# Kernel tuning notes

Hardware: AMD Instinct MI355X
Metric: run time of the kernel (lower is better)

## Reference

```python
import jax, jax.numpy as jnp
import numpy as np

N_NODES = 100000
IN_DIM = 128
OUT_DIM = 128
N_EDGES = 1000000
ALPHA = 0.2  # LeakyReLU negative slope


def _xavier(key, shape):
    gain = 1.414
    bound = gain * np.sqrt(6.0 / (shape[0] + shape[1]))
    return jax.random.uniform(key, shape, jnp.float32, -bound, bound)


def setup_inputs() -> dict:
    key = jax.random.key(0)
    ks = jax.random.split(key, 10)
    return {
        "disease_feats": jax.random.normal(ks[0], (N_NODES, IN_DIM), jnp.float32),
        "gene_feats": jax.random.normal(ks[1], (N_NODES, IN_DIM), jnp.float32),
        "chemical_feats": jax.random.normal(ks[2], (N_NODES, IN_DIM), jnp.float32),
        "species_feats": jax.random.normal(ks[3], (N_NODES, IN_DIM), jnp.float32),
        "trans_adj_list": jax.random.randint(ks[4], (4, N_EDGES), 0, N_NODES, jnp.int32),
        "P_disease": _xavier(ks[5], (IN_DIM, OUT_DIM)),
        "P_gene": _xavier(ks[6], (IN_DIM, OUT_DIM)),
        "P_chemical": _xavier(ks[7], (IN_DIM, OUT_DIM)),
        "P_species": _xavier(ks[8], (IN_DIM, OUT_DIM)),
        "W_GDCD": _xavier(ks[9], (4 * OUT_DIM, OUT_DIM)),
    }


def reference(disease_feats, gene_feats, chemical_feats, species_feats,
              trans_adj_list, P_disease, P_gene, P_chemical, P_species, W_GDCD):
    # pattern_name == 'GDCD'
    f_disease = disease_feats @ P_disease      # [N, D]
    f_gene = gene_feats @ P_gene
    f_chemical = chemical_feats @ P_chemical
    f_species = species_feats @ P_species      # computed as in original (unused for GDCD output)
    concat = jnp.concatenate([
        f_disease[trans_adj_list[0]],          # [E, D]
        f_disease[trans_adj_list[1]],
        f_gene[trans_adj_list[2]],
        f_chemical[trans_adj_list[3]],
    ], axis=1)                                 # [E, 4D]
    instance = jax.nn.leaky_relu(concat @ W_GDCD, negative_slope=ALPHA)
    return instance
```

## Files before the change

kernel.cpp:

```cpp
#include <hip/hip_runtime.h>
#include <hip/hip_fp16.h>


#define DIM 128
#define ALPHA 0.2f

__global__ __launch_bounds__(128) void compute_M(
    const float* __restrict__ Pd, const float* __restrict__ Pg,
    const float* __restrict__ Pc, const float* __restrict__ W,
    float* __restrict__ M) {
    const int i = blockIdx.x;
    const int k = blockIdx.y;
    const int j = threadIdx.x;
    const float* P = (k < 2) ? Pd : (k == 2 ? Pg : Pc);
    __shared__ float prow[DIM];
    prow[j] = P[i * DIM + j];
    __syncthreads();
    const float* Wb = W + k * DIM * DIM;
    float acc = 0.f;
#pragma unroll 8
    for (int t = 0; t < DIM; ++t)
        acc = fmaf(prow[t], Wb[t * DIM + j], acc);
    M[(k * DIM + i) * DIM + j] = acc;
}

#define BM 64
#define BK 32
__global__ __launch_bounds__(256) void node_gemm(
    const float* __restrict__ Fd, const float* __restrict__ Fg,
    const float* __restrict__ Fc, const float* __restrict__ M,
    __half* __restrict__ H, int nNodes) {
    const int k = blockIdx.y;
    const float* F = (k < 2) ? Fd : (k == 2 ? Fg : Fc);
    const float* Mk = M + k * DIM * DIM;
    __half* Hk = H + (size_t)k * nNodes * DIM;
    const int row0 = blockIdx.x * BM;

    __shared__ float As[BM][BK + 1];
    __shared__ float Bs[BK][DIM];

    const int t = threadIdx.x;
    const int tc = t & 15;
    const int tr = t >> 4;

    float acc[4][8];
#pragma unroll
    for (int i = 0; i < 4; ++i)
#pragma unroll
        for (int j = 0; j < 8; ++j) acc[i][j] = 0.f;

    for (int kk = 0; kk < DIM; kk += BK) {
#pragma unroll
        for (int q = 0; q < 2; ++q) {
            int l = q * 256 + t;
            int r = l >> 3;
            int c4 = l & 7;
            int grow = row0 + r;
            float4 v = make_float4(0.f, 0.f, 0.f, 0.f);
            if (grow < nNodes)
                v = *reinterpret_cast<const float4*>(F + (size_t)grow * DIM + kk + c4 * 4);
            As[r][c4 * 4 + 0] = v.x;
            As[r][c4 * 4 + 1] = v.y;
            As[r][c4 * 4 + 2] = v.z;
            As[r][c4 * 4 + 3] = v.w;
        }
#pragma unroll
        for (int q = 0; q < 4; ++q) {
            int l = q * 256 + t;
            int r = l >> 5;
            int c4 = l & 31;
            *reinterpret_cast<float4*>(&Bs[r][c4 * 4]) =
                *reinterpret_cast<const float4*>(Mk + (size_t)(kk + r) * DIM + c4 * 4);
        }
        __syncthreads();
#pragma unroll
        for (int kki = 0; kki < BK; ++kki) {
            float a[4];
#pragma unroll
            for (int i = 0; i < 4; ++i) a[i] = As[tr * 4 + i][kki];
            float4 b0 = *reinterpret_cast<float4*>(&Bs[kki][tc * 4]);
            float4 b1 = *reinterpret_cast<float4*>(&Bs[kki][64 + tc * 4]);
#pragma unroll
            for (int i = 0; i < 4; ++i) {
                acc[i][0] = fmaf(a[i], b0.x, acc[i][0]);
                acc[i][1] = fmaf(a[i], b0.y, acc[i][1]);
                acc[i][2] = fmaf(a[i], b0.z, acc[i][2]);
                acc[i][3] = fmaf(a[i], b0.w, acc[i][3]);
                acc[i][4] = fmaf(a[i], b1.x, acc[i][4]);
                acc[i][5] = fmaf(a[i], b1.y, acc[i][5]);
                acc[i][6] = fmaf(a[i], b1.z, acc[i][6]);
                acc[i][7] = fmaf(a[i], b1.w, acc[i][7]);
            }
        }
        __syncthreads();
    }
#pragma unroll
    for (int i = 0; i < 4; ++i) {
        int row = row0 + tr * 4 + i;
        if (row < nNodes) {
            union { __half2 h[4]; uint2 u[2]; } p;
            p.h[0] = __floats2half2_rn(acc[i][0], acc[i][1]);
            p.h[1] = __floats2half2_rn(acc[i][2], acc[i][3]);
            p.h[2] = __floats2half2_rn(acc[i][4], acc[i][5]);
            p.h[3] = __floats2half2_rn(acc[i][6], acc[i][7]);
            *reinterpret_cast<uint2*>(Hk + (size_t)row * DIM + tc * 4) = p.u[0];
            *reinterpret_cast<uint2*>(Hk + (size_t)row * DIM + 64 + tc * 4) = p.u[1];
        }
    }
}

__device__ __forceinline__ float4 load_h4(const __half* __restrict__ p) {
    float2 r = *reinterpret_cast<const float2*>(p);
    const __half2* h = reinterpret_cast<const __half2*>(&r);
    float2 lo = __half22float2(h[0]);
    float2 hi = __half22float2(h[1]);
    return make_float4(lo.x, lo.y, hi.x, hi.y);
}

__global__ __launch_bounds__(256) void edge_agg(
    const int* __restrict__ adj, const __half* __restrict__ H,
    float* __restrict__ out, int nEdges, int nNodes) {
    __shared__ int idx[32];
    const int e0 = blockIdx.x * 8;
    const int t = threadIdx.x;
    if (t < 32) {
        int j = t >> 3, i = t & 7;
        int e = e0 + i;
        idx[t] = (e < nEdges) ? adj[(size_t)j * nEdges + e] : 0;
    }
    __syncthreads();
    const int i = t >> 5;
    const int c = t & 31;
    const int e = e0 + i;
    if (e >= nEdges) return;
    const size_t NND = (size_t)nNodes * DIM;
    const int a0 = idx[i], a1 = idx[8 + i], a2 = idx[16 + i], a3 = idx[24 + i];
    const float4 v0 = load_h4(H + (size_t)a0 * DIM + c * 4);
    const float4 v1 = load_h4(H + NND + (size_t)a1 * DIM + c * 4);
    const float4 v2 = load_h4(H + 2 * NND + (size_t)a2 * DIM + c * 4);
    const float4 v3 = load_h4(H + 3 * NND + (size_t)a3 * DIM + c * 4);
    float4 s;
    s.x = v0.x + v1.x + v2.x + v3.x;
    s.y = v0.y + v1.y + v2.y + v3.y;
    s.z = v0.z + v1.z + v2.z + v3.z;
    s.w = v0.w + v1.w + v2.w + v3.w;
    s.x = s.x > 0.f ? s.x : ALPHA * s.x;
    s.y = s.y > 0.f ? s.y : ALPHA * s.y;
    s.z = s.z > 0.f ? s.z : ALPHA * s.z;
    s.w = s.w > 0.f ? s.w : ALPHA * s.w;
    float* op = out + (size_t)e * DIM + c * 4;
    __builtin_nontemporal_store(s.x, op + 0);
    __builtin_nontemporal_store(s.y, op + 1);
    __builtin_nontemporal_store(s.z, op + 2);
    __builtin_nontemporal_store(s.w, op + 3);
}

extern "C" void kernel_launch(void* const* d_in, const int* in_sizes, int n_in,
                              void* d_out, int out_size, void* d_ws, size_t ws_size,
                              hipStream_t stream) {
    const float* Fd = (const float*)d_in[0];
    const float* Fg = (const float*)d_in[1];
    const float* Fc = (const float*)d_in[2];
    const int*   adj = (const int*)d_in[4];
    const float* Pd = (const float*)d_in[5];
    const float* Pg = (const float*)d_in[6];
    const float* Pc = (const float*)d_in[7];
    const float* W  = (const float*)d_in[9];
    float* out = (float*)d_out;

    const int nNodes = in_sizes[0] / DIM;
    const int nEdges = in_sizes[4] / 4;

    float* ws_f = (float*)d_ws;
    float* M = ws_f;
    __half* H = reinterpret_cast<__half*>(ws_f + 4 * DIM * DIM);

    compute_M<<<dim3(DIM, 4), DIM, 0, stream>>>(Pd, Pg, Pc, W, M);

    dim3 g2((nNodes + BM - 1) / BM, 4);
    node_gemm<<<g2, 256, 0, stream>>>(Fd, Fg, Fc, M, H, nNodes);

    int edgeBlocks = (nEdges + 7) / 8;
    edge_agg<<<edgeBlocks, 256, 0, stream>>>(adj, H, out, nEdges, nNodes);
}
```

Before: 891.9 us.

## Use fp16 MFMA for node projection GEMM with transposed half-precision weights

```diff
diff --git a/kernel.cpp b/kernel.cpp
--- a/kernel.cpp
+++ b/kernel.cpp
@@ -5,10 +5,13 @@
 #define DIM 128
 #define ALPHA 0.2f
 
+typedef _Float16 half8 __attribute__((ext_vector_type(8)));
+typedef float    f32x4 __attribute__((ext_vector_type(4)));
+
 __global__ __launch_bounds__(128) void compute_M(
     const float* __restrict__ Pd, const float* __restrict__ Pg,
     const float* __restrict__ Pc, const float* __restrict__ W,
-    float* __restrict__ M) {
+    _Float16* __restrict__ MhT) {
     const int i = blockIdx.x;
     const int k = blockIdx.y;
     const int j = threadIdx.x;
@@ -21,90 +24,85 @@
 #pragma unroll 8
     for (int t = 0; t < DIM; ++t)
         acc = fmaf(prow[t], Wb[t * DIM + j], acc);
-    M[(k * DIM + i) * DIM + j] = acc;
+    MhT[(size_t)k * DIM * DIM + (size_t)j * DIM + i] = (_Float16)acc;
 }
 
-#define BM 64
-#define BK 32
-__global__ __launch_bounds__(256) void node_gemm(
+#define LDAP 136
+__global__ __launch_bounds__(256) void node_gemm_mfma(
     const float* __restrict__ Fd, const float* __restrict__ Fg,
-    const float* __restrict__ Fc, const float* __restrict__ M,
-    __half* __restrict__ H, int nNodes) {
-    const int k = blockIdx.y;
+    const float* __restrict__ Fc, const _Float16* __restrict__ MhT,
+    _Float16* __restrict__ H, int nNodes) {
+    const int k = blockIdx.z;
     const float* F = (k < 2) ? Fd : (k == 2 ? Fg : Fc);
-    const float* Mk = M + k * DIM * DIM;
-    __half* Hk = H + (size_t)k * nNodes * DIM;
-    const int row0 = blockIdx.x * BM;
+    const _Float16* MhTk = MhT + (size_t)k * DIM * DIM;
+    _Float16* Hk = H + (size_t)k * nNodes * DIM;
+    const int row0 = blockIdx.x * 128;
+    const int chalf = blockIdx.y;
 
-    __shared__ float As[BM][BK + 1];
-    __shared__ float Bs[BK][DIM];
+    __shared__ _Float16 As[128 * LDAP];
+    __shared__ _Float16 Bs[64 * LDAP];
 
     const int t = threadIdx.x;
-    const int tc = t & 15;
-    const int tr = t >> 4;
 
-    float acc[4][8];
 #pragma unroll
-    for (int i = 0; i < 4; ++i)
-#pragma unroll
-        for (int j = 0; j < 8; ++j) acc[i][j] = 0.f;
-
-    for (int kk = 0; kk < DIM; kk += BK) {
-#pragma unroll
-        for (int q = 0; q < 2; ++q) {
-            int l = q * 256 + t;
-            int r = l >> 3;
-            int c4 = l & 7;
-            int grow = row0 + r;
-            float4 v = make_float4(0.f, 0.f, 0.f, 0.f);
-            if (grow < nNodes)
-                v = *reinterpret_cast<const float4*>(F + (size_t)grow * DIM + kk + c4 * 4);
-            As[r][c4 * 4 + 0] = v.x;
-            As[r][c4 * 4 + 1] = v.y;
-            As[r][c4 * 4 + 2] = v.z;
-            As[r][c4 * 4 + 3] = v.w;
-        }
-#pragma unroll
-        for (int q = 0; q < 4; ++q) {
-            int l = q * 256 + t;
-            int r = l >> 5;
-            int c4 = l & 31;
-            *reinterpret_cast<float4*>(&Bs[r][c4 * 4]) =
-                *reinterpret_cast<const float4*>(Mk + (size_t)(kk + r) * DIM + c4 * 4);
-        }
-        __syncthreads();
-#pragma unroll
-        for (int kki = 0; kki < BK; ++kki) {
-            float a[4];
-#pragma unroll
-            for (int i = 0; i < 4; ++i) a[i] = As[tr * 4 + i][kki];
-            float4 b0 = *reinterpret_cast<float4*>(&Bs[kki][tc * 4]);
-            float4 b1 = *reinterpret_cast<float4*>(&Bs[kki][64 + tc * 4]);
-#pragma unroll
-            for (int i = 0; i < 4; ++i) {
-                acc[i][0] = fmaf(a[i], b0.x, acc[i][0]);
-                acc[i][1] = fmaf(a[i], b0.y, acc[i][1]);
-                acc[i][2] = fmaf(a[i], b0.z, acc[i][2]);
-                acc[i][3] = fmaf(a[i], b0.w, acc[i][3]);
-                acc[i][4] = fmaf(a[i], b1.x, acc[i][4]);
-                acc[i][5] = fmaf(a[i], b1.y, acc[i][5]);
-                acc[i][6] = fmaf(a[i], b1.z, acc[i][6]);
-                acc[i][7] = fmaf(a[i], b1.w, acc[i][7]);
-            }
-        }
-        __syncthreads();
+    for (int q = 0; q < 16; ++q) {
+        int idx = q * 256 + t;
+        int r = idx >> 5;
+        int c4 = idx & 31;
+        int grow = row0 + r;
+        float4 v = make_float4(0.f, 0.f, 0.f, 0.f);
+        if (grow < nNodes)
+            v = *reinterpret_cast<const float4*>(F + (size_t)grow * DIM + c4 * 4);
+        _Float16* dst = &As[r * LDAP + c4 * 4];
+        dst[0] = (_Float16)v.x; dst[1] = (_Float16)v.y;
+        dst[2] = (_Float16)v.z; dst[3] = (_Float16)v.w;
     }
 #pragma unroll
-    for (int i = 0; i < 4; ++i) {
-        int row = row0 + tr * 4 + i;
-        if (row < nNodes) {
-            union { __half2 h[4]; uint2 u[2]; } p;
-            p.h[0] = __floats2half2_rn(acc[i][0], acc[i][1]);
-            p.h[1] = __floats2half2_rn(acc[i][2], acc[i][3]);
-            p.h[2] = __floats2half2_rn(acc[i][4], acc[i][5]);
-            p.h[3] = __floats2half2_rn(acc[i][6], acc[i][7]);
-            *reinterpret_cast<uint2*>(Hk + (size_t)row * DIM + tc * 4) = p.u[0];
-            *reinterpret_cast<uint2*>(Hk + (size_t)row * DIM + 64 + tc * 4) = p.u[1];
+    for (int q = 0; q < 8; ++q) {
+        int idx = q * 256 + t;
+        int r = idx >> 5;
+        int k4 = idx & 31;
+        uint2 v = *reinterpret_cast<const uint2*>(
+            MhTk + (size_t)(chalf * 64 + r) * DIM + k4 * 4);
+        *reinterpret_cast<uint2*>(&Bs[r * LDAP + k4 * 4]) = v;
+    }
+    __syncthreads();
+
+    const int lane = t & 63;
+    const int w = t >> 6;
+    const int R0 = w * 32;
+    const int lane16 = lane & 15;
+    const int lgrp = lane >> 4;
+
+    f32x4 acc[2][4];
+#pragma unroll
+    for (int rt = 0; rt < 2; ++rt)
+#pragma unroll
+        for (int ct = 0; ct < 4; ++ct) acc[rt][ct] = (f32x4)0.f;
+
+#pragma unroll
+    for (int kk = 0; kk < 4; ++kk) {
+        half8 a0 = *reinterpret_cast<half8*>(&As[(R0 + lane16) * LDAP + kk * 32 + lgrp * 8]);
+        half8 a1 = *reinterpret_cast<half8*>(&As[(R0 + 16 + lane16) * LDAP + kk * 32 + lgrp * 8]);
+#pragma unroll
+        for (int ct = 0; ct < 4; ++ct) {
+            half8 b = *reinterpret_cast<half8*>(&Bs[(ct * 16 + lane16) * LDAP + kk * 32 + lgrp * 8]);
+            acc[0][ct] = __builtin_amdgcn_mfma_f32_16x16x32_f16(a0, b, acc[0][ct], 0, 0, 0);
+            acc[1][ct] = __builtin_amdgcn_mfma_f32_16x16x32_f16(a1, b, acc[1][ct], 0, 0, 0);
+        }
+    }
+
+#pragma unroll
+    for (int rt = 0; rt < 2; ++rt) {
+#pragma unroll
+        for (int ct = 0; ct < 4; ++ct) {
+            int gcol = chalf * 64 + ct * 16 + lane16;
+#pragma unroll
+            for (int j = 0; j < 4; ++j) {
+                int grow = row0 + R0 + rt * 16 + lgrp * 4 + j;
+                if (grow < nNodes)
+                    Hk[(size_t)grow * DIM + gcol] = (_Float16)acc[rt][ct][j];
+            }
         }
     }
 }
@@ -171,15 +169,14 @@
     const int nNodes = in_sizes[0] / DIM;
     const int nEdges = in_sizes[4] / 4;
 
-    float* ws_f = (float*)d_ws;
-    float* M = ws_f;
-    __half* H = reinterpret_cast<__half*>(ws_f + 4 * DIM * DIM);
+    _Float16* MhT = (_Float16*)d_ws;
+    _Float16* H = MhT + 4 * DIM * DIM;
 
-    compute_M<<<dim3(DIM, 4), DIM, 0, stream>>>(Pd, Pg, Pc, W, M);
+    compute_M<<<dim3(DIM, 4), DIM, 0, stream>>>(Pd, Pg, Pc, W, MhT);
 
-    dim3 g2((nNodes + BM - 1) / BM, 4);
-    node_gemm<<<g2, 256, 0, stream>>>(Fd, Fg, Fc, M, H, nNodes);
+    dim3 g2((nNodes + 127) / 128, 2, 4);
+    node_gemm_mfma<<<g2, 256, 0, stream>>>(Fd, Fg, Fc, MhT, H, nNodes);
 
     int edgeBlocks = (nEdges + 7) / 8;
-    edge_agg<<<edgeBlocks, 256, 0, stream>>>(adj, H, out, nEdges, nNodes);
+    edge_agg<<<edgeBlocks, 256, 0, stream>>>(adj, (const __half*)H, out, nEdges, nNodes);
 }
```

Measured after the change: 838.2 us. 1.06x faster.
